# Performance work log

Hardware: AMD Instinct MI355X
Metric: run time of the kernel (lower is better)

The kernel has to match this reference:

```python
import jax, jax.numpy as jnp
import numpy as np

# Static config (matches init_kwargs)
N = 1024        # node_num
F = 64          # input_dim (window length)
D = 64          # dim == embed_dim (heads=1)
TOPK = 20
B = 64
EPS = 1e-5      # BatchNorm eps
NEG_SLOPE = 0.2 # GraphLayer leaky_relu slope


def setup_inputs() -> dict:
    key = jax.random.key(0)
    ks = jax.random.split(key, 12)
    s = lambda fan: 1.0 / np.sqrt(fan)
    inp = {
        'data': jax.random.normal(ks[0], (B, N, F), jnp.float32),
        'org_edge_index': jax.random.randint(ks[1], (2, 2048), 0, N),
        'embedding': jax.random.normal(ks[2], (N, D), jnp.float32) * s(D),   # nn.Embedding(node_num, dim), xavier-ish
        'lin_w': jax.random.normal(ks[3], (F, D), jnp.float32) * s(F),       # GraphLayer lin (bias=False)
        'att_i': jax.random.normal(ks[4], (D,), jnp.float32) * s(D),
        'att_j': jax.random.normal(ks[5], (D,), jnp.float32) * s(D),
        'att_em_i': jax.random.normal(ks[6], (D,), jnp.float32) * s(D),
        'att_em_j': jax.random.normal(ks[7], (D,), jnp.float32) * s(D),
        'gnn_bias': jnp.zeros((D,), jnp.float32),
        'bn1_gamma': jnp.ones((D,), jnp.float32),  # GNNLayer.bn
        'bn1_beta': jnp.zeros((D,), jnp.float32),
        'bn2_gamma': jnp.ones((D,), jnp.float32),  # bn_outlayer_in
        'bn2_beta': jnp.zeros((D,), jnp.float32),
        'out_w': jax.random.normal(ks[8], (D, 1), jnp.float32) * s(D),       # OutLayer Linear(dim, 1)
        'out_b': jnp.zeros((1,), jnp.float32),
    }
    return inp


def _batchnorm(x, gamma, beta, axes):
    # training-mode BatchNorm: batch statistics over `axes`, per-feature affine
    mu = jnp.mean(x, axis=axes, keepdims=True)
    var = jnp.var(x, axis=axes, keepdims=True)
    return gamma * (x - mu) * jax.lax.rsqrt(var + EPS) + beta


def reference(data, org_edge_index, embedding, lin_w, att_i, att_j, att_em_i,
              att_em_j, gnn_bias, bn1_gamma, bn1_beta, bn2_gamma, bn2_beta,
              out_w, out_b):
    # --- dynamic graph construction from embedding cosine similarity ---
    w = jax.lax.stop_gradient(embedding)          # weights_arr.detach()
    nrm = jnp.linalg.norm(w, axis=-1)
    cos = (w @ w.T) / jnp.clip(nrm[:, None] * nrm[None, :], 1e-10)
    _, topi = jax.lax.top_k(cos, TOPK)            # [N, TOPK] neighbors j of each target i
    # (torch code drops edges whose cos value is exactly 0 -- measure-zero with
    #  random embeddings; edge count stays N*TOPK. Self edge i->i is always in topk,
    #  matching remove_self_loops + add_self_loops.)

    # --- GraphLayer (GAT-style, heads=1, concat=False, aggr='add') ---
    xl = jnp.einsum('bnf,fd->bnd', data, lin_w)   # linear transform, [B,N,D]
    xj = xl[:, topi]                               # gather neighbor feats [B,N,TOPK,D]
    ej = embedding[topi]                           # neighbor embeddings [N,TOPK,D]
    # alpha = <key_i, att_i||att_em_i> + <key_j, att_j||att_em_j>
    score = (xl @ att_i)[:, :, None] \
          + (embedding @ att_em_i)[None, :, None] \
          + jnp.einsum('bnkd,d->bnk', xj, att_j) \
          + (ej @ att_em_j)[None]                  # [B,N,TOPK]
    alpha = jax.nn.softmax(jax.nn.leaky_relu(score, NEG_SLOPE), axis=-1)
    gnn = jnp.einsum('bnk,bnkd->bnd', alpha, xj) + gnn_bias

    # GNNLayer.bn: BatchNorm1d over B*N samples, D channels
    gnn = _batchnorm(gnn, bn1_gamma, bn1_beta, axes=(0, 1))

    # --- readout ---
    out = gnn * embedding[None]                    # mul with node embedding
    out = jax.nn.relu(_batchnorm(out, bn2_gamma, bn2_beta, axes=(0, 1)))
    # dropout(0.2) -> identity (eval)
    pred = (out @ out_w + out_b).reshape(B, N)     # OutLayer: Linear(D, 1)
    return pred, out
```

## Files before the change

kernel.cpp:

```cpp
#include <hip/hip_runtime.h>

#define NN 1024
#define KK 20
#define BN 65536
#define NEG_SLOPE 0.2f

typedef unsigned short u16;
typedef unsigned int u32;
typedef unsigned long long u64;
typedef __attribute__((ext_vector_type(8))) short bf8;
typedef __attribute__((ext_vector_type(4))) float f32x4;

__device__ __forceinline__ float bf2f(u16 h) {
    return __uint_as_float(((u32)h) << 16);
}
__device__ __forceinline__ u16 f2bf(float f) {
    u32 u = __float_as_uint(f);
    u32 lsb = (u >> 16) & 1u;
    u += 0x7fffu + lsb;
    return (u16)(u >> 16);
}
__device__ __forceinline__ void up2(u32 w, float& a, float& b) {
    a = __uint_as_float(w << 16);
    b = __uint_as_float(w & 0xffff0000u);
}
__device__ __forceinline__ bool is_bf(const void* g1) {
    return *(const u32*)g1 == 0x3F803F80u;
}
template <bool BF>
__device__ __forceinline__ float ldf(const void* p, size_t i) {
    if (BF) return bf2f(((const u16*)p)[i]);
    return ((const float*)p)[i];
}
template <bool BF>
__device__ __forceinline__ void stf(void* p, size_t i, float v) {
    if (BF) ((u16*)p)[i] = f2bf(v);
    else ((float*)p)[i] = v;
}
template <bool BF>
__device__ __forceinline__ void ldf2(const void* p, size_t pairidx, float& a, float& b) {
    if (BF) {
        u32 w = ((const u32*)p)[pairidx];
        up2(w, a, b);
    } else {
        float2 v = ((const float2*)p)[pairidx];
        a = v.x;
        b = v.y;
    }
}

template <bool BF>
__device__ void k1a_body(const void* emb, const void* aei, const void* aej,
                         u16* nwH, u16* nwL, float* e_i, float* e_j, float* stats) {
    int tid = threadIdx.x;
    if (blockIdx.x == 0) {
        for (int s = tid; s < 448; s += 256) stats[s] = 0.f;
    }
    int lane = tid & 63, wave = tid >> 6;
    int n = blockIdx.x * 4 + wave;
    float v = ldf<BF>(emb, n * 64 + lane);
    float s2 = v * v;
    float si = v * ldf<BF>(aei, lane);
    float sj = v * ldf<BF>(aej, lane);
#pragma unroll
    for (int off = 32; off; off >>= 1) {
        s2 += __shfl_xor(s2, off, 64);
        si += __shfl_xor(si, off, 64);
        sj += __shfl_xor(sj, off, 64);
    }
    float rq = rsqrtf(fmaxf(s2, 1e-20f));
    float x = v * rq;
    u16 h = f2bf(x);
    nwH[n * 64 + lane] = h;
    nwL[n * 64 + lane] = f2bf(x - bf2f(h));
    if (lane == 0) { e_i[n] = si; e_j[n] = sj; }
}
__global__ __launch_bounds__(256) void k1a_norm(const void* emb, const void* aei, const void* aej,
                                                const void* probe, u16* nwH, u16* nwL,
                                                float* e_i, float* e_j, float* stats) {
    if (is_bf(probe)) k1a_body<true>(emb, aei, aej, nwH, nwL, e_i, e_j, stats);
    else k1a_body<false>(emb, aei, aej, nwH, nwL, e_i, e_j, stats);
}

__global__ __launch_bounds__(256) void k1b_gram(const u16* __restrict__ nwH,
                                                const u16* __restrict__ nwL,
                                                float* __restrict__ G) {
    int tid = threadIdx.x;
    int lane = tid & 63, wave = tid >> 6;
    int c = lane & 15, quad = lane >> 4;
    int rowblk = blockIdx.x >> 4, colblk = blockIdx.x & 15;
    int arow = rowblk * 64 + wave * 16 + c;
    bf8 aH[2], aL[2];
#pragma unroll
    for (int s = 0; s < 2; ++s) {
        aH[s] = *(const bf8*)(nwH + (size_t)arow * 64 + s * 32 + quad * 8);
        aL[s] = *(const bf8*)(nwL + (size_t)arow * 64 + s * 32 + quad * 8);
    }
    f32x4 acc[4] = {{0.f, 0.f, 0.f, 0.f}, {0.f, 0.f, 0.f, 0.f}, {0.f, 0.f, 0.f, 0.f}, {0.f, 0.f, 0.f, 0.f}};
#pragma unroll
    for (int t = 0; t < 4; ++t) {
        int bnode = colblk * 64 + t * 16 + c;
#pragma unroll
        for (int s = 0; s < 2; ++s) {
            bf8 bH = *(const bf8*)(nwH + (size_t)bnode * 64 + s * 32 + quad * 8);
            bf8 bL = *(const bf8*)(nwL + (size_t)bnode * 64 + s * 32 + quad * 8);
            acc[t] = __builtin_amdgcn_mfma_f32_16x16x32_bf16(aH[s], bH, acc[t], 0, 0, 0);
            acc[t] = __builtin_amdgcn_mfma_f32_16x16x32_bf16(aH[s], bL, acc[t], 0, 0, 0);
            acc[t] = __builtin_amdgcn_mfma_f32_16x16x32_bf16(aL[s], bH, acc[t], 0, 0, 0);
        }
    }
#pragma unroll
    for (int t = 0; t < 4; ++t) {
#pragma unroll
        for (int reg = 0; reg < 4; ++reg) {
            int row = rowblk * 64 + wave * 16 + quad * 4 + reg;
            G[(size_t)row * 1024 + colblk * 64 + t * 16 + c] = acc[t][reg];
        }
    }
}

__global__ __launch_bounds__(256) void k1c_select(const float* __restrict__ G, int* __restrict__ topi) {
    int lane = threadIdx.x & 63, wave = threadIdx.x >> 6;
    int n = blockIdx.x * 4 + wave;
    const f32x4* gp = (const f32x4*)(G + (size_t)n * 1024 + lane * 16);
    f32x4 v0 = gp[0], v1 = gp[1], v2 = gp[2], v3 = gp[3];
    float c[16] = {v0.x, v0.y, v0.z, v0.w, v1.x, v1.y, v1.z, v1.w,
                   v2.x, v2.y, v2.z, v2.w, v3.x, v3.y, v3.z, v3.w};
    u32 o[16];
#pragma unroll
    for (int j = 0; j < 16; ++j) {
        u32 u = __float_as_uint(c[j]);
        o[j] = u ^ (u32)(((int)u >> 31) | 0x80000000);
    }
    unsigned mask = 0u;
    int keep = 0;
    for (int r = 0; r < KK; ++r) {
        u32 bo = 0u;
        int bj = 0;
#pragma unroll
        for (int j = 0; j < 16; ++j) {
            bool t = !((mask >> j) & 1u) && o[j] > bo;
            bo = t ? o[j] : bo;
            bj = t ? j : bj;
        }
        u64 key = ((u64)bo << 32) | (u32)(~(u32)(lane * 16 + bj));
#pragma unroll
        for (int off = 32; off; off >>= 1) {
            u64 ok = __shfl_xor((unsigned long long)key, off, 64);
            key = ok > key ? ok : key;
        }
        int bm = (int)((~(u32)key) & 1023u);
        if ((bm >> 4) == lane) mask |= 1u << (bm & 15);
        if (lane == r) keep = bm;
    }
    if (lane < KK) topi[n * KK + lane] = keep;
}

template <bool BF>
__device__ void k2_body(const void* data, const void* lin_w, const void* att_i, const void* att_j,
                        u16* xl, float* a_i, float* a_j) {
    __shared__ u16 Bl[64 * 72];
    __shared__ u16 Ct[64 * 72];
    int tid = threadIdx.x;
    {
        int k = tid >> 2, n0 = (tid & 3) * 16;
        if (BF) {
            const u16* lw = (const u16*)lin_w;
#pragma unroll
            for (int i = 0; i < 16; ++i) Bl[(n0 + i) * 72 + k] = lw[k * 64 + n0 + i];
        } else {
            const float* lw = (const float*)lin_w;
#pragma unroll
            for (int i = 0; i < 16; ++i) Bl[(n0 + i) * 72 + k] = f2bf(lw[k * 64 + n0 + i]);
        }
    }
    __syncthreads();
    int lane = tid & 63, wave = tid >> 6;
    int c = lane & 15, quad = lane >> 4;
    int m0 = blockIdx.x * 64 + wave * 16;
    size_t row = (size_t)(m0 + c);
    f32x4 acc[4] = {{0.f, 0.f, 0.f, 0.f}, {0.f, 0.f, 0.f, 0.f}, {0.f, 0.f, 0.f, 0.f}, {0.f, 0.f, 0.f, 0.f}};
#pragma unroll
    for (int s = 0; s < 2; ++s) {
        bf8 a;
        if (BF) {
            a = *(const bf8*)((const u16*)data + row * 64 + s * 32 + quad * 8);
        } else {
            const float* dp = (const float*)data + row * 64 + s * 32 + quad * 8;
            f32x4 x0 = *(const f32x4*)dp;
            f32x4 x1 = *(const f32x4*)(dp + 4);
            a[0] = (short)f2bf(x0.x); a[1] = (short)f2bf(x0.y);
            a[2] = (short)f2bf(x0.z); a[3] = (short)f2bf(x0.w);
            a[4] = (short)f2bf(x1.x); a[5] = (short)f2bf(x1.y);
            a[6] = (short)f2bf(x1.z); a[7] = (short)f2bf(x1.w);
        }
#pragma unroll
        for (int t = 0; t < 4; ++t) {
            bf8 b = *(const bf8*)&Bl[(t * 16 + c) * 72 + s * 32 + quad * 8];
            acc[t] = __builtin_amdgcn_mfma_f32_16x16x32_bf16(a, b, acc[t], 0, 0, 0);
        }
    }
    float wi[4], wj[4];
#pragma unroll
    for (int t = 0; t < 4; ++t) {
        wi[t] = ldf<BF>(att_i, t * 16 + c);
        wj[t] = ldf<BF>(att_j, t * 16 + c);
    }
    float ai4[4] = {0.f, 0.f, 0.f, 0.f}, aj4[4] = {0.f, 0.f, 0.f, 0.f};
#pragma unroll
    for (int t = 0; t < 4; ++t) {
#pragma unroll
        for (int reg = 0; reg < 4; ++reg) {
            float v = acc[t][reg];
            Ct[(wave * 16 + quad * 4 + reg) * 72 + t * 16 + c] = f2bf(v);
            ai4[reg] += v * wi[t];
            aj4[reg] += v * wj[t];
        }
    }
#pragma unroll
    for (int reg = 0; reg < 4; ++reg) {
#pragma unroll
        for (int off = 1; off < 16; off <<= 1) {
            ai4[reg] += __shfl_xor(ai4[reg], off, 64);
            aj4[reg] += __shfl_xor(aj4[reg], off, 64);
        }
    }
    if (c == 0) {
#pragma unroll
        for (int reg = 0; reg < 4; ++reg) {
            a_i[m0 + quad * 4 + reg] = ai4[reg];
            a_j[m0 + quad * 4 + reg] = aj4[reg];
        }
    }
    __syncthreads();
    {
        int r = tid >> 2, seg = tid & 3;
        uint4 v0 = *(const uint4*)&Ct[r * 72 + seg * 16];
        uint4 v1 = *(const uint4*)&Ct[r * 72 + seg * 16 + 8];
        uint4* dst = (uint4*)xl + ((size_t)(blockIdx.x * 64 + r) * 8 + seg * 2);
        dst[0] = v0;
        dst[1] = v1;
    }
}
__global__ __launch_bounds__(256) void k2_mfma(const void* data, const void* lin_w,
                                               const void* att_i, const void* att_j, const void* probe,
                                               u16* xl, float* a_i, float* a_j) {
    if (is_bf(probe)) k2_body<true>(data, lin_w, att_i, att_j, xl, a_i, a_j);
    else k2_body<false>(data, lin_w, att_i, att_j, xl, a_i, a_j);
}

template <bool BF>
__device__ void k3_body(const u16* xl, const float* a_i, const float* a_j, const float* e_i,
                        const float* e_j, const int* topi, const void* emb, const void* gnn_bias,
                        void* dout, float* stats) {
    __shared__ float ps[4][7][64];
    __shared__ uint2 sp[4][2][KK];
    int tid = threadIdx.x;
    int lane = tid & 63, wave = tid >> 6;
    int half = lane >> 5, hl = lane & 31;
    int b = blockIdx.x & 63;
    int jj = blockIdx.x >> 6;
    int wig = jj * 4 + wave;
    int n0 = wig * 16;
    const u32* xb = (const u32*)xl + ((size_t)b << 15);
    float bias0, bias1;
    ldf2<BF>(gnn_bias, hl, bias0, bias1);
    float se[14];
#pragma unroll
    for (int s = 0; s < 14; ++s) se[s] = 0.f;
    for (int ii = 0; ii < 8; ++ii) {
        int n = n0 + 2 * ii + half;
        int pair = (b << 10) + n;
        int t = 0;
        float sc = -3e38f;
        if (hl < KK) {
            t = topi[n * KK + hl];
            sc = a_i[pair] + e_i[n] + a_j[(b << 10) + t] + e_j[t];
            sc = sc >= 0.f ? sc : NEG_SLOPE * sc;
        }
        float m = sc;
#pragma unroll
        for (int off = 16; off; off >>= 1) m = fmaxf(m, __shfl_xor(m, off, 32));
        float p = (hl < KK) ? __expf(sc - m) : 0.f;
        float S = p;
#pragma unroll
        for (int off = 16; off; off >>= 1) S += __shfl_xor(S, off, 32);
        if (hl < KK) {
            uint2 v; v.x = (u32)t; v.y = __float_as_uint(p / S);
            sp[wave][half][hl] = v;
        }
        float acc0 = 0.f, acc1 = 0.f;
#pragma unroll
        for (int k = 0; k < KK; ++k) {
            uint2 v = sp[wave][half][k];
            u32 w = xb[(v.x << 5) + hl];
            float alpha = __uint_as_float(v.y);
            acc0 += alpha * __uint_as_float(w << 16);
            acc1 += alpha * __uint_as_float(w & 0xffff0000u);
        }
        acc0 += bias0;
        acc1 += bias1;
        if (BF) {
            u32 pk = (u32)f2bf(acc0) | ((u32)f2bf(acc1) << 16);
            ((u32*)dout)[(BN >> 1) + pair * 32 + hl] = pk;
        } else {
            float2 v2; v2.x = acc0; v2.y = acc1;
            ((float2*)dout)[(BN >> 1) + pair * 32 + hl] = v2;
        }
        float em0, em1;
        ldf2<BF>(emb, n * 32 + hl, em0, em1);
        se[0] += acc0; se[1] += acc1;
        se[2] += acc0 * acc0; se[3] += acc1 * acc1;
        float ge0 = acc0 * em0, ge1 = acc1 * em1;
        se[4] += ge0; se[5] += ge1;
        se[6] += ge0 * ge0; se[7] += ge1 * ge1;
        se[8] += ge0 * em0; se[9] += ge1 * em1;
        se[10] += em0; se[11] += em1;
        se[12] += em0 * em0; se[13] += em1 * em1;
    }
#pragma unroll
    for (int s = 0; s < 14; ++s) se[s] += __shfl_xor(se[s], 32, 64);
    if (half == 0) {
#pragma unroll
        for (int s = 0; s < 7; ++s) {
            ps[wave][s][2 * hl] = se[2 * s];
            ps[wave][s][2 * hl + 1] = se[2 * s + 1];
        }
    }
    __syncthreads();
    const float* pf = &ps[0][0][0];
    for (int q = tid; q < 448; q += 256) {
        atomicAdd(&stats[q], pf[q] + pf[448 + q] + pf[896 + q] + pf[1344 + q]);
    }
}
__global__ __launch_bounds__(256) void k3_gnn(const u16* xl, const float* a_i, const float* a_j,
                                              const float* e_i, const float* e_j, const int* topi,
                                              const void* emb, const void* gnn_bias, const void* probe,
                                              void* dout, float* stats) {
    if (is_bf(probe)) k3_body<true>(xl, a_i, a_j, e_i, e_j, topi, emb, gnn_bias, dout, stats);
    else k3_body<false>(xl, a_i, a_j, e_i, e_j, topi, emb, gnn_bias, dout, stats);
}

template <bool BF>
__device__ void k5_body(const void* emb, const float* stats, const void* g1, const void* b1,
                        const void* g2, const void* b2, const void* out_w, const void* out_b,
                        void* dout) {
    int lane = threadIdx.x & 63;
    float P, Q, R;
    {
        int d = lane;
        double inv = 1.0 / 65536.0;
        double S1 = stats[d], S2 = stats[64 + d], T1 = stats[128 + d], T2 = stats[192 + d];
        double T3 = stats[256 + d], U1 = stats[320 + d], U2 = stats[384 + d];
        double mu1 = S1 * inv;
        double var1 = S2 * inv - mu1 * mu1;
        if (var1 < 0.0) var1 = 0.0;
        double r1 = 1.0 / sqrt(var1 + 1e-5);
        double A = (double)ldf<BF>(g1, d) * r1;
        double C = (double)ldf<BF>(b1, d) - A * mu1;
        double E1 = A * T1 + C * U1;
        double mu2 = E1 * inv;
        double E2 = A * A * T2 + 2.0 * A * C * T3 + C * C * U2;
        double var2 = E2 * inv - mu2 * mu2;
        if (var2 < 0.0) var2 = 0.0;
        double r2 = 1.0 / sqrt(var2 + 1e-5);
        double g2r2 = (double)ldf<BF>(g2, d) * r2;
        P = (float)(g2r2 * A);
        Q = (float)(g2r2 * C);
        R = (float)((double)ldf<BF>(b2, d) - g2r2 * mu2);
    }
    int gw = (blockIdx.x * 256 + threadIdx.x) >> 6;
    float wo = ldf<BF>(out_w, lane);
    float ob = ldf<BF>(out_b, 0);
    int row0 = gw * 8;
    for (int i = 0; i < 8; ++i) {
        int row = row0 + i;
        int n = row & 1023;
        size_t oi = (size_t)BN + (size_t)row * 64 + lane;
        float g = ldf<BF>(dout, oi);
        float em = ldf<BF>(emb, n * 64 + lane);
        float o = fmaxf(P * g * em + Q * em + R, 0.f);
        stf<BF>(dout, oi, o);
        float p = o * wo;
#pragma unroll
        for (int off = 32; off; off >>= 1) p += __shfl_xor(p, off, 64);
        if (lane == 0) stf<BF>(dout, row, p + ob);
    }
}
__global__ __launch_bounds__(256) void k5_out(const void* emb, const float* stats, const void* g1,
                                              const void* b1, const void* g2, const void* b2,
                                              const void* out_w, const void* out_b, void* dout) {
    if (is_bf(g1)) k5_body<true>(emb, stats, g1, b1, g2, b2, out_w, out_b, dout);
    else k5_body<false>(emb, stats, g1, b1, g2, b2, out_w, out_b, dout);
}

extern "C" void kernel_launch(void* const* d_in, const int* in_sizes, int n_in,
                              void* d_out, int out_size, void* d_ws, size_t ws_size,
                              hipStream_t stream) {
    const void* data = d_in[0];
    const void* emb = d_in[2];
    const void* lin_w = d_in[3];
    const void* att_i = d_in[4];
    const void* att_j = d_in[5];
    const void* att_em_i = d_in[6];
    const void* att_em_j = d_in[7];
    const void* gnn_bias = d_in[8];
    const void* bn1_g = d_in[9];
    const void* bn1_b = d_in[10];
    const void* bn2_g = d_in[11];
    const void* bn2_b = d_in[12];
    const void* out_w = d_in[13];
    const void* out_b = d_in[14];

    char* ws = (char*)d_ws;
    float* a_i = (float*)ws;
    float* a_j = a_i + 65536;
    float* e_i = a_j + 65536;
    float* e_j = e_i + 1024;
    float* stats = e_j + 1024;
    int* topi = (int*)(stats + 448);
    u16* xl = (u16*)(topi + 20480);
    u16* nwH = xl + 4194304;
    u16* nwL = nwH + 65536;
    float* G = (float*)(nwL + 65536);

    k1a_norm<<<256, 256, 0, stream>>>(emb, att_em_i, att_em_j, bn1_g, nwH, nwL, e_i, e_j, stats);
    k1b_gram<<<256, 256, 0, stream>>>(nwH, nwL, G);
    k1c_select<<<256, 256, 0, stream>>>(G, topi);
    k2_mfma<<<1024, 256, 0, stream>>>(data, lin_w, att_i, att_j, bn1_g, xl, a_i, a_j);
    k3_gnn<<<1024, 256, 0, stream>>>(xl, a_i, a_j, e_i, e_j, topi, emb, gnn_bias, bn1_g, d_out, stats);
    k5_out<<<2048, 256, 0, stream>>>(emb, stats, bn1_g, bn1_b, bn2_g, bn2_b, out_w, out_b, d_out);
}
```

Before: 171.3 us.

## Split GNN aggregation into separate alpha softmax and gather kernels

Moves the per-node attention score and softmax computation into its own kernel that writes (index, alpha) pairs to a workspace buffer. The aggregation kernel then reads precomputed alphas, handles half as many nodes per wave, and launches twice as many blocks for more parallelism. The batch-invariant embedding statistics move into the norm kernel, and stats zeroing becomes a memset. The trade is an extra launch plus a 10 MB intermediate round trip through global memory.

```diff
diff --git a/kernel.cpp b/kernel.cpp
--- a/kernel.cpp
+++ b/kernel.cpp
@@ -52,13 +52,13 @@
 template <bool BF>
 __device__ void k1a_body(const void* emb, const void* aei, const void* aej,
                          u16* nwH, u16* nwL, float* e_i, float* e_j, float* stats) {
+    __shared__ float sme[4][64], sm2[4][64];
     int tid = threadIdx.x;
-    if (blockIdx.x == 0) {
-        for (int s = tid; s < 448; s += 256) stats[s] = 0.f;
-    }
     int lane = tid & 63, wave = tid >> 6;
     int n = blockIdx.x * 4 + wave;
     float v = ldf<BF>(emb, n * 64 + lane);
+    sme[wave][lane] = v;
+    sm2[wave][lane] = v * v;
     float s2 = v * v;
     float si = v * ldf<BF>(aei, lane);
     float sj = v * ldf<BF>(aej, lane);
@@ -74,6 +74,15 @@
     nwH[n * 64 + lane] = h;
     nwL[n * 64 + lane] = f2bf(x - bf2f(h));
     if (lane == 0) { e_i[n] = si; e_j[n] = sj; }
+    __syncthreads();
+    if (tid < 64) {
+        float u1 = sme[0][tid] + sme[1][tid] + sme[2][tid] + sme[3][tid];
+        atomicAdd(&stats[320 + tid], 64.f * u1);
+    } else if (tid < 128) {
+        int d = tid - 64;
+        float u2 = sm2[0][d] + sm2[1][d] + sm2[2][d] + sm2[3][d];
+        atomicAdd(&stats[384 + d], 64.f * u2);
+    }
 }
 __global__ __launch_bounds__(256) void k1a_norm(const void* emb, const void* aei, const void* aej,
                                                 const void* probe, u16* nwH, u16* nwL,
@@ -249,11 +258,44 @@
     else k2_body<false>(data, lin_w, att_i, att_j, xl, a_i, a_j);
 }
 
-template <bool BF>
-__device__ void k3_body(const u16* xl, const float* a_i, const float* a_j, const float* e_i,
-                        const float* e_j, const int* topi, const void* emb, const void* gnn_bias,
-                        void* dout, float* stats) {
-    __shared__ float ps[4][7][64];
+__global__ __launch_bounds__(256) void k3a_alpha(const int* __restrict__ topi,
+                                                 const float* __restrict__ a_i,
+                                                 const float* __restrict__ a_j,
+                                                 const float* __restrict__ e_i,
+                                                 const float* __restrict__ e_j,
+                                                 uint2* __restrict__ alphaT) {
+    int tid = threadIdx.x;
+    int lane = tid & 63, wave = tid >> 6;
+    int half = lane >> 5, hl = lane & 31;
+    int b = blockIdx.x & 63;
+    int n = (blockIdx.x >> 6) * 8 + wave * 2 + half;
+    int pair = (b << 10) + n;
+    int t = 0;
+    float sc = -3e38f;
+    if (hl < KK) {
+        t = topi[n * KK + hl];
+        sc = a_i[pair] + e_i[n] + a_j[(b << 10) + t] + e_j[t];
+        sc = sc >= 0.f ? sc : NEG_SLOPE * sc;
+    }
+    float m = sc;
+#pragma unroll
+    for (int off = 16; off; off >>= 1) m = fmaxf(m, __shfl_xor(m, off, 32));
+    float p = (hl < KK) ? __expf(sc - m) : 0.f;
+    float S = p;
+#pragma unroll
+    for (int off = 16; off; off >>= 1) S += __shfl_xor(S, off, 32);
+    if (hl < KK) {
+        uint2 v;
+        v.x = (u32)t;
+        v.y = __float_as_uint(p / S);
+        alphaT[(size_t)pair * KK + hl] = v;
+    }
+}
+
+template <bool BF>
+__device__ void k3b_body(const u16* xl, const uint2* alphaT, const void* emb,
+                         const void* gnn_bias, void* dout, float* stats) {
+    __shared__ float ps[4][5][64];
     __shared__ uint2 sp[4][2][KK];
     int tid = threadIdx.x;
     int lane = tid & 63, wave = tid >> 6;
@@ -261,34 +303,17 @@
     int b = blockIdx.x & 63;
     int jj = blockIdx.x >> 6;
     int wig = jj * 4 + wave;
-    int n0 = wig * 16;
+    int n0 = wig * 8;
     const u32* xb = (const u32*)xl + ((size_t)b << 15);
     float bias0, bias1;
     ldf2<BF>(gnn_bias, hl, bias0, bias1);
-    float se[14];
-#pragma unroll
-    for (int s = 0; s < 14; ++s) se[s] = 0.f;
-    for (int ii = 0; ii < 8; ++ii) {
+    float se[10];
+#pragma unroll
+    for (int s = 0; s < 10; ++s) se[s] = 0.f;
+    for (int ii = 0; ii < 4; ++ii) {
         int n = n0 + 2 * ii + half;
         int pair = (b << 10) + n;
-        int t = 0;
-        float sc = -3e38f;
-        if (hl < KK) {
-            t = topi[n * KK + hl];
-            sc = a_i[pair] + e_i[n] + a_j[(b << 10) + t] + e_j[t];
-            sc = sc >= 0.f ? sc : NEG_SLOPE * sc;
-        }
-        float m = sc;
-#pragma unroll
-        for (int off = 16; off; off >>= 1) m = fmaxf(m, __shfl_xor(m, off, 32));
-        float p = (hl < KK) ? __expf(sc - m) : 0.f;
-        float S = p;
-#pragma unroll
-        for (int off = 16; off; off >>= 1) S += __shfl_xor(S, off, 32);
-        if (hl < KK) {
-            uint2 v; v.x = (u32)t; v.y = __float_as_uint(p / S);
-            sp[wave][half][hl] = v;
-        }
+        if (hl < KK) sp[wave][half][hl] = alphaT[(size_t)pair * KK + hl];
         float acc0 = 0.f, acc1 = 0.f;
 #pragma unroll
         for (int k = 0; k < KK; ++k) {
@@ -315,30 +340,27 @@
         se[4] += ge0; se[5] += ge1;
         se[6] += ge0 * ge0; se[7] += ge1 * ge1;
         se[8] += ge0 * em0; se[9] += ge1 * em1;
-        se[10] += em0; se[11] += em1;
-        se[12] += em0 * em0; se[13] += em1 * em1;
-    }
-#pragma unroll
-    for (int s = 0; s < 14; ++s) se[s] += __shfl_xor(se[s], 32, 64);
+    }
+#pragma unroll
+    for (int s = 0; s < 10; ++s) se[s] += __shfl_xor(se[s], 32, 64);
     if (half == 0) {
 #pragma unroll
-        for (int s = 0; s < 7; ++s) {
+        for (int s = 0; s < 5; ++s) {
             ps[wave][s][2 * hl] = se[2 * s];
             ps[wave][s][2 * hl + 1] = se[2 * s + 1];
         }
     }
     __syncthreads();
     const float* pf = &ps[0][0][0];
-    for (int q = tid; q < 448; q += 256) {
-        atomicAdd(&stats[q], pf[q] + pf[448 + q] + pf[896 + q] + pf[1344 + q]);
-    }
-}
-__global__ __launch_bounds__(256) void k3_gnn(const u16* xl, const float* a_i, const float* a_j,
-                                              const float* e_i, const float* e_j, const int* topi,
-                                              const void* emb, const void* gnn_bias, const void* probe,
-                                              void* dout, float* stats) {
-    if (is_bf(probe)) k3_body<true>(xl, a_i, a_j, e_i, e_j, topi, emb, gnn_bias, dout, stats);
-    else k3_body<false>(xl, a_i, a_j, e_i, e_j, topi, emb, gnn_bias, dout, stats);
+    for (int q = tid; q < 320; q += 256) {
+        atomicAdd(&stats[q], pf[q] + pf[320 + q] + pf[640 + q] + pf[960 + q]);
+    }
+}
+__global__ __launch_bounds__(256) void k3b_gnn(const u16* xl, const uint2* alphaT, const void* emb,
+                                               const void* gnn_bias, const void* probe,
+                                               void* dout, float* stats) {
+    if (is_bf(probe)) k3b_body<true>(xl, alphaT, emb, gnn_bias, dout, stats);
+    else k3b_body<false>(xl, alphaT, emb, gnn_bias, dout, stats);
 }
 
 template <bool BF>
@@ -423,11 +445,14 @@
     u16* nwH = xl + 4194304;
     u16* nwL = nwH + 65536;
     float* G = (float*)(nwL + 65536);
-
+    uint2* alphaT = (uint2*)(G + 1048576);
+
+    hipMemsetAsync(stats, 0, 448 * sizeof(float), stream);
     k1a_norm<<<256, 256, 0, stream>>>(emb, att_em_i, att_em_j, bn1_g, nwH, nwL, e_i, e_j, stats);
     k1b_gram<<<256, 256, 0, stream>>>(nwH, nwL, G);
     k1c_select<<<256, 256, 0, stream>>>(G, topi);
     k2_mfma<<<1024, 256, 0, stream>>>(data, lin_w, att_i, att_j, bn1_g, xl, a_i, a_j);
-    k3_gnn<<<1024, 256, 0, stream>>>(xl, a_i, a_j, e_i, e_j, topi, emb, gnn_bias, bn1_g, d_out, stats);
+    k3a_alpha<<<8192, 256, 0, stream>>>(topi, a_i, a_j, e_i, e_j, alphaT);
+    k3b_gnn<<<2048, 256, 0, stream>>>(xl, alphaT, emb, gnn_bias, bn1_g, d_out, stats);
     k5_out<<<2048, 256, 0, stream>>>(emb, stats, bn1_g, bn1_b, bn2_g, bn2_b, out_w, out_b, d_out);
 }
```

Result: slower. 206.4 us (+20.5%).
